# Kernel optimization log

Measured on AMD Instinct MI355X. Metric: run time of the kernel, lower is better.

The kernel has to match this reference:

```python
import math
import jax, jax.numpy as jnp
import numpy as np

BN_EPS = 1e-5

def _lrelu(x, s):
    return jnp.where(x >= 0, x, s * x)

def _bn(x, g, b):
    # BatchNorm2d in train mode (torch default): biased batch stats over (B,H,W)
    mu = jnp.mean(x, axis=(0, 2, 3), keepdims=True)
    var = jnp.mean((x - mu) ** 2, axis=(0, 2, 3), keepdims=True)
    return (x - mu) / jnp.sqrt(var + BN_EPS) * g[None, :, None, None] + b[None, :, None, None]

def _knn(x, x2, k):
    # x: [B,d,P], x2: [B,d,S] -> idx [B,k,S]: k nearest points of x for each column of x2
    inner = -2.0 * jnp.einsum('bdp,bds->bps', x, x2)
    xx = jnp.sum(x ** 2, axis=1)[:, :, None]    # [B,P,1]
    xx2 = jnp.sum(x2 ** 2, axis=1)[:, None, :]  # [B,1,S]
    d = -xx - inner - xx2                        # [B,P,S], larger = closer
    _, idx = jax.lax.top_k(jnp.transpose(d, (0, 2, 1)), k)  # [B,S,k]
    return jnp.transpose(idx, (0, 2, 1))         # [B,k,S]

def _gather_nb(X, idx, s, k):
    # faithful to torch gether_neibour, including its flat-reshape layout
    B, C, P = X.shape
    base = jnp.arange(B)[:, None, None] * P
    flat = (idx + base).reshape(-1)
    Xt = jnp.transpose(X, (0, 2, 1)).reshape(B * P, C)
    return Xt[flat].reshape(B, s, k, C)

def _c2d(x, W, b):
    return jnp.einsum('oc,bcpk->bopk', W, x) + b[None, :, None, None]

def _c1d(x, W, b):
    return jnp.einsum('oc,bcp->bop', W, x) + b[None, :, None]

def _forward(x, W_pos, b_pos, g2, be2, W_conv, b_conv, g1, be1, W_a1, b_a1, W_a2, b_a2, W_b1, b_b1, W_b2, b_b2, num_points):
    B, C, P = x.shape
    k = 8
    s = num_points
    # ---- Dynamic_sampling_M: uniform mesh over (x,y) bbox, snap to nearest event ----
    L = int(math.ceil(math.sqrt(s)))
    m = jnp.arange(L, dtype=x.dtype) / L
    m01 = jnp.tile(m[None, :], (L, 1)).reshape(1, 1, L * L)
    m02 = jnp.tile(m[:, None], (1, L)).reshape(1, 1, L * L)
    mesh = jnp.broadcast_to(jnp.concatenate([m01, m02], axis=1), (B, 2, L * L))
    Px = jax.lax.stop_gradient(x[:, :2, :])  # knn runs under torch.no_grad
    mn = Px.min(axis=2, keepdims=True)
    mx = Px.max(axis=2, keepdims=True)
    PS = mesh * (mx - mn) + mn
    idx0 = _knn(Px, PS, 1)                                   # [B,1,L*L]
    sp = _gather_nb(x, idx0, L * L, 1)[:, :, 0, :].transpose(0, 2, 1)  # [B,C,s]
    idx = _knn(jax.lax.stop_gradient(x[:, :3, :]), jax.lax.stop_gradient(sp[:, :3, :]), k)  # [B,k,s]
    x1 = jnp.transpose(_gather_nb(x, idx, s, k), (0, 3, 1, 2))  # [B,C,s,k]
    # ---- positional encoding ----
    PA = x1[:, :3, :, :]
    PC = x1[:, :3, :, 0:1]
    diff = PA - PC
    sq = jnp.sum(diff ** 2, axis=1, keepdims=True)
    temp = jnp.where(sq > 0, jnp.sqrt(jnp.where(sq > 0, sq, 1.0)), 0.0)
    PEmb = jnp.concatenate([PA, jnp.broadcast_to(PC, PA.shape), diff, temp], axis=1)  # [B,10,s,k]
    PEmb = _lrelu(_bn(_c2d(PEmb, W_pos, b_pos), g2, be2), 0.2)
    x_ = _lrelu(_bn(_c2d(x1[:, :4, :, :], W_conv, b_conv), g1, be1), 0.2)
    feat = jnp.concatenate([x_, PEmb], axis=1)  # [B,64,s,k]
    att = _c2d(_lrelu(_c2d(feat, W_a1, b_a1), 0.2), W_a2, b_a2)  # [B,1,s,k]
    att = jax.nn.softmax(att, axis=-1)
    feat = jnp.sum(feat * att, axis=-1)  # [B,64,s]
    Fea1 = _c1d(feat, W_b1, b_b1)
    Fea2 = _c1d(x1[:, :4, :, 0], W_b2, b_b2)
    out = _lrelu(Fea1 + Fea2, 0.01)
    return jnp.concatenate([x1[:, :5, :, 0], out], axis=1)  # [B,69,s]

def setup_inputs() -> dict:
    key = jax.random.key(0)
    ks = jax.random.split(key, 8)
    B, C, P = 2, 5, 16384
    num_points = 4096  # perfect square required by the mesh sampler
    outc, inc, h = 64, 4, 32
    w = lambda k_, shape: jax.random.normal(k_, shape, jnp.float32) * 0.05
    x = jax.random.normal(ks[0], (B, C, P), jnp.float32)
    return dict(
        x=x,
        W_pos=w(ks[1], (h, 10)), b_pos=jnp.zeros((h,), jnp.float32),
        g2=jnp.ones((h,), jnp.float32), be2=jnp.zeros((h,), jnp.float32),
        W_conv=w(ks[2], (h, inc)), b_conv=jnp.zeros((h,), jnp.float32),
        g1=jnp.ones((h,), jnp.float32), be1=jnp.zeros((h,), jnp.float32),
        W_a1=w(ks[3], (32, outc)), b_a1=jnp.zeros((32,), jnp.float32),
        W_a2=w(ks[4], (1, 32)), b_a2=jnp.zeros((1,), jnp.float32),
        W_b1=w(ks[5], (outc, outc)), b_b1=jnp.zeros((outc,), jnp.float32),
        W_b2=w(ks[6], (outc, inc)), b_b2=jnp.zeros((outc,), jnp.float32),
        num_points=num_points,
    )

def reference(x, W_pos, b_pos, g2, be2, W_conv, b_conv, g1, be1, W_a1, b_a1, W_a2, b_a2, W_b1, b_b1, W_b2, b_b2, num_points):
    return _forward(x, W_pos, b_pos, g2, be2, W_conv, b_conv, g1, be1, W_a1, b_a1, W_a2, b_a2, W_b1, b_b1, W_b2, b_b2, num_points)
```

## Files before the change

kernel.cpp:

```cpp
#include <hip/hip_runtime.h>
#include <math.h>

#define B_ 2
#define P_ 16384
#define C_ 5
#define S_ 4096
#define KNN_ 8
#define L_ 64

typedef unsigned short u16;
typedef unsigned int u32;

__device__ int   g_idxk[B_ * KNN_ * S_];
__device__ float g_sums[128];

__device__ __forceinline__ float bf2f(u16 u) {
  union { u32 i; float f; } c; c.i = ((u32)u) << 16; return c.f;
}
__device__ __forceinline__ u16 f2bf(float f) {
  union { float f; u32 i; } c; c.f = f;
  u32 r = c.i + 0x7fffu + ((c.i >> 16) & 1u);
  return (u16)(r >> 16);
}
__device__ __forceinline__ float ldany(const void* p, int i, int f32) {
  return f32 ? ((const float*)p)[i] : bf2f(((const u16*)p)[i]);
}

__device__ __forceinline__ double packkey(float d, int idx) {
  u32 bits = __float_as_uint(d);
  u32 key = bits ^ ((u32)(((int)bits) >> 31) | 0x80000000u);
  int hi = (int)(0x3FF00000u | (key >> 12));
  int lo = (int)((key << 20) | ((u32)(16383 - idx) << 6));
  return __hiloint2double(hi, lo);
}
__device__ __forceinline__ int keyidx(double w) {
  return 16383 - (int)(((u32)__double2loint(w) >> 6) & 16383u);
}
__device__ __forceinline__ void cmpswap(double& a, double& b) {
  double hi = fmax(a, b), lo = fmin(a, b);
  a = hi; b = lo;
}
__device__ __forceinline__ void flush8(double* a, double* k) {
  cmpswap(k[0], k[1]); cmpswap(k[2], k[3]); cmpswap(k[4], k[5]); cmpswap(k[6], k[7]);
  cmpswap(k[0], k[2]); cmpswap(k[1], k[3]); cmpswap(k[4], k[6]); cmpswap(k[5], k[7]);
  cmpswap(k[1], k[2]); cmpswap(k[5], k[6]);
  cmpswap(k[0], k[4]); cmpswap(k[1], k[5]); cmpswap(k[2], k[6]); cmpswap(k[3], k[7]);
  cmpswap(k[2], k[4]); cmpswap(k[3], k[5]);
  cmpswap(k[1], k[2]); cmpswap(k[3], k[4]); cmpswap(k[5], k[6]);
  a[0] = fmax(a[0], k[7]); a[1] = fmax(a[1], k[6]);
  a[2] = fmax(a[2], k[5]); a[3] = fmax(a[3], k[4]);
  a[4] = fmax(a[4], k[3]); a[5] = fmax(a[5], k[2]);
  a[6] = fmax(a[6], k[1]); a[7] = fmax(a[7], k[0]);
  cmpswap(a[0], a[4]); cmpswap(a[1], a[5]); cmpswap(a[2], a[6]); cmpswap(a[3], a[7]);
  cmpswap(a[0], a[2]); cmpswap(a[1], a[3]); cmpswap(a[4], a[6]); cmpswap(a[5], a[7]);
  cmpswap(a[0], a[1]); cmpswap(a[2], a[3]); cmpswap(a[4], a[5]); cmpswap(a[6], a[7]);
}

__device__ __forceinline__ int chk_bad(const void* p, int n, int tid) {
  int bad = 0;
  for (int i = tid; i < n; i += 256) {
    float f = bf2f(((const u16*)p)[i]);
    if (!(f == f) || fabsf(f) > 1024.0f) bad = 1;
  }
  return bad;
}

__global__ __launch_bounds__(256, 4) void k_knn(const void* __restrict__ xv) {
  __shared__ float4 s4[1024];
  __shared__ int sidx[8];
  __shared__ int sbad;
  __shared__ float sred[16];
  int tid = threadIdx.x;
  if (blockIdx.x == 0 && tid < 128) g_sums[tid] = 0.0f;
  int l = tid & 63, g = tid >> 6;
  int sg0 = blockIdx.x * 8 + g * 2;
  int b = sg0 >> 12;
  int base0 = b * C_ * P_, base1 = base0 + P_, base2 = base1 + P_;

  if (tid == 0) sbad = 0;
  __syncthreads();
  if (chk_bad(xv, 1024, tid)) atomicOr(&sbad, 1);
  __syncthreads();
  const int f32 = sbad;

  float mn0 = INFINITY, mx0 = -INFINITY, mn1 = INFINITY, mx1 = -INFINITY;
  for (int p = tid; p < P_; p += 256) {
    float v0 = ldany(xv, base0 + p, f32);
    float v1 = ldany(xv, base1 + p, f32);
    mn0 = fminf(mn0, v0); mx0 = fmaxf(mx0, v0);
    mn1 = fminf(mn1, v1); mx1 = fmaxf(mx1, v1);
  }
  for (int off = 32; off; off >>= 1) {
    mn0 = fminf(mn0, __shfl_down(mn0, off)); mx0 = fmaxf(mx0, __shfl_down(mx0, off));
    mn1 = fminf(mn1, __shfl_down(mn1, off)); mx1 = fmaxf(mx1, __shfl_down(mx1, off));
  }
  if (l == 0) {
    sred[g * 4 + 0] = mn0; sred[g * 4 + 1] = mx0;
    sred[g * 4 + 2] = mn1; sred[g * 4 + 3] = mx1;
  }
  __syncthreads();
  mn0 = fminf(fminf(sred[0], sred[4]), fminf(sred[8], sred[12]));
  mx0 = fmaxf(fmaxf(sred[1], sred[5]), fmaxf(sred[9], sred[13]));
  mn1 = fminf(fminf(sred[2], sred[6]), fminf(sred[10], sred[14]));
  mx1 = fmaxf(fmaxf(sred[3], sred[7]), fmaxf(sred[11], sred[15]));

  float ps0[2], ps1[2], xx2[2], best[2]; int bestp[2];
#pragma unroll
  for (int qq = 0; qq < 2; ++qq) {
    int s = (sg0 + qq) & (S_ - 1);
    float mm0 = (float)(s & (L_ - 1)) * 0.015625f;
    float mm1 = (float)(s >> 6) * 0.015625f;
    ps0[qq] = __fadd_rn(__fmul_rn(mm0, __fsub_rn(mx0, mn0)), mn0);
    ps1[qq] = __fadd_rn(__fmul_rn(mm1, __fsub_rn(mx1, mn1)), mn1);
    xx2[qq] = __fadd_rn(__fmul_rn(ps0[qq], ps0[qq]), __fmul_rn(ps1[qq], ps1[qq]));
    best[qq] = -INFINITY; bestp[qq] = 0x7fffffff;
  }
  for (int c = 0; c < 16; ++c) {
    __syncthreads();
    for (int i = tid; i < 1024; i += 256) {
      int gi = c * 1024 + i;
      float a0 = ldany(xv, base0 + gi, f32);
      float a1 = ldany(xv, base1 + gi, f32);
      float xx = __fadd_rn(__fmul_rn(a0, a0), __fmul_rn(a1, a1));
      s4[i] = make_float4(a0, a1, xx, 0.0f);
    }
    __syncthreads();
    for (int t = 0; t < 16; ++t) {
      float4 v = s4[t * 64 + l];
      int ix = c * 1024 + t * 64 + l;
#pragma unroll
      for (int qq = 0; qq < 2; ++qq) {
        float dot = __fadd_rn(__fmul_rn(v.x, ps0[qq]), __fmul_rn(v.y, ps1[qq]));
        float inner = __fmul_rn(-2.0f, dot);
        float d = __fsub_rn(__fsub_rn(-v.z, inner), xx2[qq]);
        bool gt = d > best[qq];
        best[qq] = gt ? d : best[qq];
        bestp[qq] = gt ? ix : bestp[qq];
      }
    }
  }
#pragma unroll
  for (int qq = 0; qq < 2; ++qq) {
    float v = best[qq]; int ix = bestp[qq];
    for (int m = 1; m < 64; m <<= 1) {
      float ov = __shfl_xor(v, m, 64); int op = __shfl_xor(ix, m, 64);
      if (ov > v || (ov == v && op < ix)) { v = ov; ix = op; }
    }
    if (l == 0) sidx[g * 2 + qq] = ix;
  }
  __syncthreads();

  float q0[2], q1[2], q2[2], xx3q[2];
  double acc[2][8], kb[2][8];
#pragma unroll
  for (int qq = 0; qq < 2; ++qq) {
    int qi = sidx[g * 2 + qq] & (P_ - 1);
    q0[qq] = ldany(xv, base0 + qi, f32);
    q1[qq] = ldany(xv, base1 + qi, f32);
    q2[qq] = ldany(xv, base2 + qi, f32);
    xx3q[qq] = __fadd_rn(__fadd_rn(__fmul_rn(q0[qq], q0[qq]), __fmul_rn(q1[qq], q1[qq])),
                         __fmul_rn(q2[qq], q2[qq]));
#pragma unroll
    for (int k = 0; k < 8; ++k) acc[qq][k] = -1.0;
  }
  for (int c = 0; c < 16; ++c) {
    __syncthreads();
    for (int i = tid; i < 1024; i += 256) {
      int gi = c * 1024 + i;
      float a0 = ldany(xv, base0 + gi, f32);
      float a1 = ldany(xv, base1 + gi, f32);
      float a2 = ldany(xv, base2 + gi, f32);
      float xx = __fadd_rn(__fadd_rn(__fmul_rn(a0, a0), __fmul_rn(a1, a1)), __fmul_rn(a2, a2));
      s4[i] = make_float4(a0, a1, a2, xx);
    }
    __syncthreads();
#pragma unroll
    for (int t = 0; t < 16; ++t) {
      float4 v = s4[t * 64 + l];
      int ix = c * 1024 + t * 64 + l;
#pragma unroll
      for (int qq = 0; qq < 2; ++qq) {
        float dot = __fadd_rn(__fadd_rn(__fmul_rn(v.x, q0[qq]), __fmul_rn(v.y, q1[qq])),
                              __fmul_rn(v.z, q2[qq]));
        float inner = __fmul_rn(-2.0f, dot);
        float d = __fsub_rn(__fsub_rn(-v.w, inner), xx3q[qq]);
        kb[qq][t & 7] = packkey(d, ix);
      }
      if ((t & 7) == 7) {
        flush8(acc[0], kb[0]);
        flush8(acc[1], kb[1]);
      }
    }
  }
  double wk[2] = {0.0, 0.0};
#pragma unroll
  for (int qq = 0; qq < 2; ++qq) {
#pragma unroll
    for (int r = 0; r < 8; ++r) {
      double w = acc[qq][0];
      for (int m = 1; m < 64; m <<= 1) w = fmax(w, __shfl_xor(w, m, 64));
      if (l == r) wk[qq] = w;
      bool cns = (acc[qq][0] == w);
#pragma unroll
      for (int k = 0; k < 7; ++k) acc[qq][k] = cns ? acc[qq][k + 1] : acc[qq][k];
      acc[qq][7] = cns ? -1.0 : acc[qq][7];
    }
  }
  if (l < 8) {
#pragma unroll
    for (int qq = 0; qq < 2; ++qq) {
      int s = (sg0 + qq) & (S_ - 1);
      g_idxk[b * 32768 + l * 4096 + s] = keyidx(wk[qq]);
    }
  }
}

__device__ __forceinline__ void elem_vals(const void* xv, int xf32, int xbase,
                                          const int* fb, int n,
                                          const float* sWpos, const float* sbpos,
                                          const float* sWconv, const float* sbconv,
                                          float* val ) {
  int p = fb[n] & (P_ - 1);
  int p0 = fb[n & ~7] & (P_ - 1);
  float xvv[4];
#pragma unroll
  for (int c = 0; c < 4; ++c) xvv[c] = ldany(xv, xbase + c * P_ + p, xf32);
  float pc[3];
#pragma unroll
  for (int c = 0; c < 3; ++c) pc[c] = ldany(xv, xbase + c * P_ + p0, xf32);
  float d0 = xvv[0] - pc[0], d1 = xvv[1] - pc[1], d2 = xvv[2] - pc[2];
  float sq = d0 * d0 + d1 * d1 + d2 * d2;
  float temp = (sq > 0.0f) ? sqrtf(sq) : 0.0f;
  float pe[10] = {xvv[0], xvv[1], xvv[2], pc[0], pc[1], pc[2], d0, d1, d2, temp};
#pragma unroll
  for (int o = 0; o < 32; ++o) {
    float acc = sbconv[o];
#pragma unroll
    for (int c = 0; c < 4; ++c) acc = fmaf(sWconv[o * 4 + c], xvv[c], acc);
    val[o] = acc;
  }
#pragma unroll
  for (int o = 0; o < 32; ++o) {
    float acc = sbpos[o];
#pragma unroll
    for (int c = 0; c < 10; ++c) acc = fmaf(sWpos[o * 10 + c], pe[c], acc);
    val[32 + o] = acc;
  }
}

__global__ __launch_bounds__(256) void k_partial(const void* __restrict__ x,
                                                 const void* __restrict__ Wpos,
                                                 const void* __restrict__ bpos,
                                                 const void* __restrict__ Wconv,
                                                 const void* __restrict__ bconv) {
  __shared__ float sWpos[320], sbpos[32], sWconv[128], sbconv[32];
  __shared__ float sacc[4][128];
  __shared__ int sbx, sbw;
  int tid = threadIdx.x;
  if (tid == 0) { sbx = 0; sbw = 0; }
  __syncthreads();
  if (chk_bad(x, 1024, tid)) atomicOr(&sbx, 1);
  if (chk_bad(Wpos, 320, tid) | chk_bad(Wconv, 128, tid)) atomicOr(&sbw, 1);
  __syncthreads();
  int xf32 = sbx, wf32 = sbw;
  for (int i2 = tid; i2 < 320; i2 += 256) sWpos[i2] = ldany(Wpos, i2, wf32);
  if (tid < 128) sWconv[tid] = ldany(Wconv, tid, wf32);
  if (tid < 32) { sbpos[tid] = ldany(bpos, tid, wf32); sbconv[tid] = ldany(bconv, tid, wf32); }
  __syncthreads();
  int t = blockIdx.x * 256 + tid;
  int b = t >> 15, n = t & 32767;
  const int* fb = g_idxk + b * 32768;
  float val[64];
  elem_vals(x, xf32, b * C_ * P_, fb, n, sWpos, sbpos, sWconv, sbconv, val);
  int wid = tid >> 6, lane = tid & 63;
#pragma unroll
  for (int c = 0; c < 64; ++c) {
    float s = val[c], q = val[c] * val[c];
    for (int off = 32; off; off >>= 1) {
      s += __shfl_down(s, off);
      q += __shfl_down(q, off);
    }
    if (lane == 0) { sacc[wid][c * 2] = s; sacc[wid][c * 2 + 1] = q; }
  }
  __syncthreads();
  if (tid < 128) {
    float v = sacc[0][tid] + sacc[1][tid] + sacc[2][tid] + sacc[3][tid];
    atomicAdd(&g_sums[tid], v);
  }
}

__global__ __launch_bounds__(256) void k_pass2(const void* __restrict__ x,
                                               const void* __restrict__ Wpos,
                                               const void* __restrict__ bpos,
                                               const void* __restrict__ Wconv,
                                               const void* __restrict__ bconv,
                                               const void* __restrict__ g1,
                                               const void* __restrict__ be1,
                                               const void* __restrict__ g2,
                                               const void* __restrict__ be2,
                                               const void* __restrict__ Wa1,
                                               const void* __restrict__ ba1,
                                               const void* __restrict__ Wa2,
                                               const void* __restrict__ ba2,
                                               const void* __restrict__ Wb1,
                                               const void* __restrict__ bb1,
                                               const void* __restrict__ Wb2,
                                               const void* __restrict__ bb2,
                                               void* __restrict__ out) {
  __shared__ float sWpos[320], sbpos[32], sWconv[128], sbconv[32];
  __shared__ float sWa1[2048], sba1[32], sWa2[32];
  __shared__ float sWb1[64 * 65];
  __shared__ float sbb1[64], sWb2[256], sbb2[64], sstats[128];
  __shared__ float sba2;
  __shared__ int sbx, sbw;
  int tid = threadIdx.x;
  if (tid == 0) { sbx = 0; sbw = 0; }
  __syncthreads();
  if (chk_bad(x, 1024, tid)) atomicOr(&sbx, 1);
  if (chk_bad(Wa1, 2048, tid) | chk_bad(Wb1, 4096, tid)) atomicOr(&sbw, 1);
  __syncthreads();
  int xf32 = sbx, wf32 = sbw;
  for (int i2 = tid; i2 < 320; i2 += 256) sWpos[i2] = ldany(Wpos, i2, wf32);
  if (tid < 128) sWconv[tid] = ldany(Wconv, tid, wf32);
  if (tid < 32) { sbpos[tid] = ldany(bpos, tid, wf32); sbconv[tid] = ldany(bconv, tid, wf32); }
  for (int i2 = tid; i2 < 2048; i2 += 256) sWa1[i2] = ldany(Wa1, i2, wf32);
  for (int i2 = tid; i2 < 4096; i2 += 256) sWb1[(i2 >> 6) * 65 + (i2 & 63)] = ldany(Wb1, i2, wf32);
  if (tid >= 32 && tid < 64) { sba1[tid - 32] = ldany(ba1, tid - 32, wf32); sWa2[tid - 32] = ldany(Wa2, tid - 32, wf32); }
  if (tid >= 64 && tid < 128) { sbb1[tid - 64] = ldany(bb1, tid - 64, wf32); sbb2[tid - 64] = ldany(bb2, tid - 64, wf32); }
  sWb2[tid] = ldany(Wb2, tid, wf32);
  if (tid == 0) sba2 = ldany(ba2, 0, wf32);
  if (tid >= 128 && tid < 192) {
    int ch = tid - 128;
    float sum = g_sums[ch * 2], sq = g_sums[ch * 2 + 1];
    float mean = sum * (1.0f / 65536.0f);
    float var = sq * (1.0f / 65536.0f) - mean * mean;
    int o = ch & 31;
    float gg = ldany(ch < 32 ? g1 : g2, o, wf32);
    float be = ldany(ch < 32 ? be1 : be2, o, wf32);
    float scale = gg / sqrtf(var + 1e-5f);
    sstats[ch * 2] = scale;
    sstats[ch * 2 + 1] = be - mean * scale;
  }
  __syncthreads();
  int g = blockIdx.x * 32 + (tid >> 3);
  int j = tid & 7;
  int b = g >> 12, i = g & (S_ - 1);
  int n = i * 8 + j;
  const int* fb = g_idxk + b * 32768;
  int xbase = b * C_ * P_;
  float feat[64];
  elem_vals(x, xf32, xbase, fb, n, sWpos, sbpos, sWconv, sbconv, feat);
#pragma unroll
  for (int c = 0; c < 64; ++c) {
    float v = fmaf(feat[c], sstats[c * 2], sstats[c * 2 + 1]);
    feat[c] = (v >= 0.f) ? v : 0.2f * v;
  }
  float att = sba2;
  for (int h = 0; h < 32; ++h) {
    float acc = sba1[h];
#pragma unroll
    for (int c = 0; c < 64; ++c) acc = fmaf(sWa1[h * 64 + c], feat[c], acc);
    acc = (acc >= 0.f) ? acc : 0.2f * acc;
    att = fmaf(sWa2[h], acc, att);
  }
  float mxv = att;
  for (int mk = 1; mk < 8; mk <<= 1) mxv = fmaxf(mxv, __shfl_xor(mxv, mk, 8));
  float e = expf(att - mxv);
  float se = e;
  for (int mk = 1; mk < 8; mk <<= 1) se += __shfl_xor(se, mk, 8);
  float a = e / se;
#pragma unroll
  for (int c = 0; c < 64; ++c) {
    float w = feat[c] * a;
    w += __shfl_xor(w, 1, 8);
    w += __shfl_xor(w, 2, 8);
    w += __shfl_xor(w, 4, 8);
    feat[c] = w;
  }
  int p0 = fb[i * 8] & (P_ - 1);
  float xc0 = ldany(x, xbase + p0, xf32);
  float xc1 = ldany(x, xbase + P_ + p0, xf32);
  float xc2 = ldany(x, xbase + 2 * P_ + p0, xf32);
  float xc3 = ldany(x, xbase + 3 * P_ + p0, xf32);
  int obase = b * 69 * S_;
#pragma unroll
  for (int oc = 0; oc < 8; ++oc) {
    int o = j * 8 + oc;
    float acc = sbb1[o];
#pragma unroll
    for (int c = 0; c < 64; ++c) acc = fmaf(sWb1[o * 65 + c], feat[c], acc);
    float acc2 = sbb2[o];
    acc2 = fmaf(sWb2[o * 4 + 0], xc0, acc2);
    acc2 = fmaf(sWb2[o * 4 + 1], xc1, acc2);
    acc2 = fmaf(sWb2[o * 4 + 2], xc2, acc2);
    acc2 = fmaf(sWb2[o * 4 + 3], xc3, acc2);
    float r = acc + acc2;
    r = (r >= 0.f) ? r : 0.01f * r;
    int oi = obase + (5 + o) * S_ + i;
    if (xf32) ((float*)out)[oi] = r; else ((u16*)out)[oi] = f2bf(r);
  }
  if (j == 0) {
#pragma unroll
    for (int c = 0; c < 5; ++c) {
      int oi = obase + c * S_ + i;
      if (xf32) ((float*)out)[oi] = ((const float*)x)[xbase + c * P_ + p0];
      else      ((u16*)out)[oi]   = ((const u16*)x)[xbase + c * P_ + p0];
    }
  }
}

extern "C" void kernel_launch(void* const* d_in, const int* in_sizes, int n_in,
                              void* d_out, int out_size, void* d_ws, size_t ws_size,
                              hipStream_t stream) {
  const void* x     = d_in[0];
  const void* Wpos  = d_in[1];
  const void* bpos  = d_in[2];
  const void* g2    = d_in[3];
  const void* be2   = d_in[4];
  const void* Wconv = d_in[5];
  const void* bconv = d_in[6];
  const void* g1    = d_in[7];
  const void* be1   = d_in[8];
  const void* Wa1   = d_in[9];
  const void* ba1   = d_in[10];
  const void* Wa2   = d_in[11];
  const void* ba2   = d_in[12];
  const void* Wb1   = d_in[13];
  const void* bb1   = d_in[14];
  const void* Wb2   = d_in[15];
  const void* bb2   = d_in[16];
  (void)d_ws; (void)ws_size; (void)in_sizes; (void)n_in;

  hipLaunchKernelGGL(k_knn, dim3(1024), dim3(256), 0, stream, x);
  hipLaunchKernelGGL(k_partial, dim3(256), dim3(256), 0, stream, x,
                     Wpos, bpos, Wconv, bconv);
  hipLaunchKernelGGL(k_pass2, dim3(256), dim3(256), 0, stream, x,
                     Wpos, bpos, Wconv, bconv, g1, be1, g2, be2,
                     Wa1, ba1, Wa2, ba2, Wb1, bb1, Wb2, bb2, d_out);
}
```

Before: 298.9 us.

## Fuse BN partial stats into kNN kernel and double-buffer point tiles

Removes the separate k_partial kernel. The kNN kernel now computes per-block BatchNorm sum and sum-of-squares partials for its own 16 neighbour features and writes them to a global partials array, and pass2 reduces those partials instead of reading atomically accumulated sums. The kNN point-tile loops are also double-buffered in shared memory: the next chunk is loaded into registers while the current one is scanned, which removes one barrier per chunk. This saves a kernel launch and a re-read of the indices, and overlaps global loads with compute. In exchange it costs more shared memory and registers in k_knn, which may reduce occupancy, and adds a serial 512-element reduction loop per thread in every pass2 block.

```diff
diff --git a/kernel.cpp b/kernel.cpp
--- a/kernel.cpp
+++ b/kernel.cpp
@@ -12,7 +12,7 @@
 typedef unsigned int u32;
 
 __device__ int   g_idxk[B_ * KNN_ * S_];
-__device__ float g_sums[128];
+__device__ float g_partials[1024 * 128];
 
 __device__ __forceinline__ float bf2f(u16 u) {
   union { u32 i; float f; } c; c.i = ((u32)u) << 16; return c.f;
@@ -65,23 +65,34 @@
   return bad;
 }
 
-__global__ __launch_bounds__(256, 4) void k_knn(const void* __restrict__ xv) {
-  __shared__ float4 s4[1024];
+__global__ __launch_bounds__(256, 4) void k_knn(const void* __restrict__ xv,
+                                                const void* __restrict__ Wpos,
+                                                const void* __restrict__ bpos,
+                                                const void* __restrict__ Wconv,
+                                                const void* __restrict__ bconv) {
+  __shared__ float4 s4[2][1024];
+  __shared__ float sWpos[320], sbpos[32], sWconv[128], sbconv[32];
+  __shared__ float sacc[4][128];
   __shared__ int sidx[8];
-  __shared__ int sbad;
+  __shared__ int sp0[8];
+  __shared__ int sbad, sbw;
   __shared__ float sred[16];
   int tid = threadIdx.x;
-  if (blockIdx.x == 0 && tid < 128) g_sums[tid] = 0.0f;
   int l = tid & 63, g = tid >> 6;
   int sg0 = blockIdx.x * 8 + g * 2;
   int b = sg0 >> 12;
   int base0 = b * C_ * P_, base1 = base0 + P_, base2 = base1 + P_;
 
-  if (tid == 0) sbad = 0;
+  if (tid == 0) { sbad = 0; sbw = 0; }
   __syncthreads();
   if (chk_bad(xv, 1024, tid)) atomicOr(&sbad, 1);
-  __syncthreads();
-  const int f32 = sbad;
+  if (chk_bad(Wpos, 320, tid) | chk_bad(Wconv, 128, tid)) atomicOr(&sbw, 1);
+  __syncthreads();
+  const int f32 = sbad, wf32 = sbw;
+
+  for (int i2 = tid; i2 < 320; i2 += 256) sWpos[i2] = ldany(Wpos, i2, wf32);
+  if (tid < 128) sWconv[tid] = ldany(Wconv, tid, wf32);
+  if (tid < 32) { sbpos[tid] = ldany(bpos, tid, wf32); sbconv[tid] = ldany(bconv, tid, wf32); }
 
   float mn0 = INFINITY, mx0 = -INFINITY, mn1 = INFINITY, mx1 = -INFINITY;
   for (int p = tid; p < P_; p += 256) {
@@ -115,18 +126,30 @@
     xx2[qq] = __fadd_rn(__fmul_rn(ps0[qq], ps0[qq]), __fmul_rn(ps1[qq], ps1[qq]));
     best[qq] = -INFINITY; bestp[qq] = 0x7fffffff;
   }
+  {
+#pragma unroll
+    for (int r = 0; r < 4; ++r) {
+      int i = r * 256 + tid;
+      float a0 = ldany(xv, base0 + i, f32);
+      float a1 = ldany(xv, base1 + i, f32);
+      float xx = __fadd_rn(__fmul_rn(a0, a0), __fmul_rn(a1, a1));
+      s4[0][i] = make_float4(a0, a1, xx, 0.0f);
+    }
+  }
+  __syncthreads();
   for (int c = 0; c < 16; ++c) {
-    __syncthreads();
-    for (int i = tid; i < 1024; i += 256) {
-      int gi = c * 1024 + i;
-      float a0 = ldany(xv, base0 + gi, f32);
-      float a1 = ldany(xv, base1 + gi, f32);
-      float xx = __fadd_rn(__fmul_rn(a0, a0), __fmul_rn(a1, a1));
-      s4[i] = make_float4(a0, a1, xx, 0.0f);
-    }
-    __syncthreads();
+    float a0r[4], a1r[4];
+    if (c < 15) {
+#pragma unroll
+      for (int r = 0; r < 4; ++r) {
+        int gi = (c + 1) * 1024 + r * 256 + tid;
+        a0r[r] = ldany(xv, base0 + gi, f32);
+        a1r[r] = ldany(xv, base1 + gi, f32);
+      }
+    }
+    const float4* cb = s4[c & 1];
     for (int t = 0; t < 16; ++t) {
-      float4 v = s4[t * 64 + l];
+      float4 v = cb[t * 64 + l];
       int ix = c * 1024 + t * 64 + l;
 #pragma unroll
       for (int qq = 0; qq < 2; ++qq) {
@@ -138,6 +161,15 @@
         bestp[qq] = gt ? ix : bestp[qq];
       }
     }
+    if (c < 15) {
+      float4* nb = s4[(c + 1) & 1];
+#pragma unroll
+      for (int r = 0; r < 4; ++r) {
+        float xx = __fadd_rn(__fmul_rn(a0r[r], a0r[r]), __fmul_rn(a1r[r], a1r[r]));
+        nb[r * 256 + tid] = make_float4(a0r[r], a1r[r], xx, 0.0f);
+      }
+    }
+    __syncthreads();
   }
 #pragma unroll
   for (int qq = 0; qq < 2; ++qq) {
@@ -163,20 +195,33 @@
 #pragma unroll
     for (int k = 0; k < 8; ++k) acc[qq][k] = -1.0;
   }
+  {
+#pragma unroll
+    for (int r = 0; r < 4; ++r) {
+      int i = r * 256 + tid;
+      float a0 = ldany(xv, base0 + i, f32);
+      float a1 = ldany(xv, base1 + i, f32);
+      float a2 = ldany(xv, base2 + i, f32);
+      float xx = __fadd_rn(__fadd_rn(__fmul_rn(a0, a0), __fmul_rn(a1, a1)), __fmul_rn(a2, a2));
+      s4[0][i] = make_float4(a0, a1, a2, xx);
+    }
+  }
+  __syncthreads();
   for (int c = 0; c < 16; ++c) {
-    __syncthreads();
-    for (int i = tid; i < 1024; i += 256) {
-      int gi = c * 1024 + i;
-      float a0 = ldany(xv, base0 + gi, f32);
-      float a1 = ldany(xv, base1 + gi, f32);
-      float a2 = ldany(xv, base2 + gi, f32);
-      float xx = __fadd_rn(__fadd_rn(__fmul_rn(a0, a0), __fmul_rn(a1, a1)), __fmul_rn(a2, a2));
-      s4[i] = make_float4(a0, a1, a2, xx);
-    }
-    __syncthreads();
+    float a0r[4], a1r[4], a2r[4];
+    if (c < 15) {
+#pragma unroll
+      for (int r = 0; r < 4; ++r) {
+        int gi = (c + 1) * 1024 + r * 256 + tid;
+        a0r[r] = ldany(xv, base0 + gi, f32);
+        a1r[r] = ldany(xv, base1 + gi, f32);
+        a2r[r] = ldany(xv, base2 + gi, f32);
+      }
+    }
+    const float4* cb = s4[c & 1];
 #pragma unroll
     for (int t = 0; t < 16; ++t) {
-      float4 v = s4[t * 64 + l];
+      float4 v = cb[t * 64 + l];
       int ix = c * 1024 + t * 64 + l;
 #pragma unroll
       for (int qq = 0; qq < 2; ++qq) {
@@ -191,6 +236,16 @@
         flush8(acc[1], kb[1]);
       }
     }
+    if (c < 15) {
+      float4* nb = s4[(c + 1) & 1];
+#pragma unroll
+      for (int r = 0; r < 4; ++r) {
+        float xx = __fadd_rn(__fadd_rn(__fmul_rn(a0r[r], a0r[r]), __fmul_rn(a1r[r], a1r[r])),
+                             __fmul_rn(a2r[r], a2r[r]));
+        nb[r * 256 + tid] = make_float4(a0r[r], a1r[r], a2r[r], xx);
+      }
+    }
+    __syncthreads();
   }
   double wk[2] = {0.0, 0.0};
 #pragma unroll
@@ -213,79 +268,46 @@
       g_idxk[b * 32768 + l * 4096 + s] = keyidx(wk[qq]);
     }
   }
-}
-
-__device__ __forceinline__ void elem_vals(const void* xv, int xf32, int xbase,
-                                          const int* fb, int n,
-                                          const float* sWpos, const float* sbpos,
-                                          const float* sWconv, const float* sbconv,
-                                          float* val ) {
-  int p = fb[n] & (P_ - 1);
-  int p0 = fb[n & ~7] & (P_ - 1);
-  float xvv[4];
-#pragma unroll
-  for (int c = 0; c < 4; ++c) xvv[c] = ldany(xv, xbase + c * P_ + p, xf32);
-  float pc[3];
-#pragma unroll
-  for (int c = 0; c < 3; ++c) pc[c] = ldany(xv, xbase + c * P_ + p0, xf32);
-  float d0 = xvv[0] - pc[0], d1 = xvv[1] - pc[1], d2 = xvv[2] - pc[2];
+
+  if (g == 0 && l < 8) sp0[l] = keyidx(wk[0]) & (P_ - 1);
+  __syncthreads();
+  double k1s = __shfl(wk[1], l & 7, 16);
+  bool active = (l < 16);
+  double myk = (l < 8) ? wk[0] : k1s;
+  int p = keyidx(myk) & (P_ - 1);
+  int p0 = sp0[l & 7];
+  float xvv[4] = {0, 0, 0, 0}, pc3[3] = {0, 0, 0};
+  if (active) {
+#pragma unroll
+    for (int cc = 0; cc < 4; ++cc) xvv[cc] = ldany(xv, base0 + cc * P_ + p, f32);
+#pragma unroll
+    for (int cc = 0; cc < 3; ++cc) pc3[cc] = ldany(xv, base0 + cc * P_ + p0, f32);
+  }
+  float d0 = xvv[0] - pc3[0], d1 = xvv[1] - pc3[1], d2 = xvv[2] - pc3[2];
   float sq = d0 * d0 + d1 * d1 + d2 * d2;
   float temp = (sq > 0.0f) ? sqrtf(sq) : 0.0f;
-  float pe[10] = {xvv[0], xvv[1], xvv[2], pc[0], pc[1], pc[2], d0, d1, d2, temp};
-#pragma unroll
-  for (int o = 0; o < 32; ++o) {
-    float acc = sbconv[o];
-#pragma unroll
-    for (int c = 0; c < 4; ++c) acc = fmaf(sWconv[o * 4 + c], xvv[c], acc);
-    val[o] = acc;
-  }
-#pragma unroll
-  for (int o = 0; o < 32; ++o) {
-    float acc = sbpos[o];
-#pragma unroll
-    for (int c = 0; c < 10; ++c) acc = fmaf(sWpos[o * 10 + c], pe[c], acc);
-    val[32 + o] = acc;
-  }
-}
-
-__global__ __launch_bounds__(256) void k_partial(const void* __restrict__ x,
-                                                 const void* __restrict__ Wpos,
-                                                 const void* __restrict__ bpos,
-                                                 const void* __restrict__ Wconv,
-                                                 const void* __restrict__ bconv) {
-  __shared__ float sWpos[320], sbpos[32], sWconv[128], sbconv[32];
-  __shared__ float sacc[4][128];
-  __shared__ int sbx, sbw;
-  int tid = threadIdx.x;
-  if (tid == 0) { sbx = 0; sbw = 0; }
-  __syncthreads();
-  if (chk_bad(x, 1024, tid)) atomicOr(&sbx, 1);
-  if (chk_bad(Wpos, 320, tid) | chk_bad(Wconv, 128, tid)) atomicOr(&sbw, 1);
-  __syncthreads();
-  int xf32 = sbx, wf32 = sbw;
-  for (int i2 = tid; i2 < 320; i2 += 256) sWpos[i2] = ldany(Wpos, i2, wf32);
-  if (tid < 128) sWconv[tid] = ldany(Wconv, tid, wf32);
-  if (tid < 32) { sbpos[tid] = ldany(bpos, tid, wf32); sbconv[tid] = ldany(bconv, tid, wf32); }
-  __syncthreads();
-  int t = blockIdx.x * 256 + tid;
-  int b = t >> 15, n = t & 32767;
-  const int* fb = g_idxk + b * 32768;
-  float val[64];
-  elem_vals(x, xf32, b * C_ * P_, fb, n, sWpos, sbpos, sWconv, sbconv, val);
-  int wid = tid >> 6, lane = tid & 63;
-#pragma unroll
-  for (int c = 0; c < 64; ++c) {
-    float s = val[c], q = val[c] * val[c];
-    for (int off = 32; off; off >>= 1) {
-      s += __shfl_down(s, off);
-      q += __shfl_down(q, off);
-    }
-    if (lane == 0) { sacc[wid][c * 2] = s; sacc[wid][c * 2 + 1] = q; }
+  float pe[10] = {xvv[0], xvv[1], xvv[2], pc3[0], pc3[1], pc3[2], d0, d1, d2, temp};
+#pragma unroll
+  for (int o = 0; o < 64; ++o) {
+    float v;
+    if (o < 32) {
+      v = sbconv[o];
+#pragma unroll
+      for (int cc = 0; cc < 4; ++cc) v = fmaf(sWconv[o * 4 + cc], xvv[cc], v);
+    } else {
+      v = sbpos[o - 32];
+#pragma unroll
+      for (int cc = 0; cc < 10; ++cc) v = fmaf(sWpos[(o - 32) * 10 + cc], pe[cc], v);
+    }
+    v = active ? v : 0.0f;
+    float s = v, q = v * v;
+    for (int m = 1; m < 16; m <<= 1) { s += __shfl_xor(s, m, 16); q += __shfl_xor(q, m, 16); }
+    if (l == 0) { sacc[g][o * 2] = s; sacc[g][o * 2 + 1] = q; }
   }
   __syncthreads();
   if (tid < 128) {
-    float v = sacc[0][tid] + sacc[1][tid] + sacc[2][tid] + sacc[3][tid];
-    atomicAdd(&g_sums[tid], v);
+    g_partials[blockIdx.x * 128 + tid] =
+        sacc[0][tid] + sacc[1][tid] + sacc[2][tid] + sacc[3][tid];
   }
 }
 
@@ -311,6 +333,7 @@
   __shared__ float sWa1[2048], sba1[32], sWa2[32];
   __shared__ float sWb1[64 * 65];
   __shared__ float sbb1[64], sWb2[256], sbb2[64], sstats[128];
+  __shared__ float sp2[2][128];
   __shared__ float sba2;
   __shared__ int sbx, sbw;
   int tid = threadIdx.x;
@@ -320,6 +343,13 @@
   if (chk_bad(Wa1, 2048, tid) | chk_bad(Wb1, 4096, tid)) atomicOr(&sbw, 1);
   __syncthreads();
   int xf32 = sbx, wf32 = sbw;
+  {
+    int slot = tid & 127, half = tid >> 7;
+    float a = 0.f;
+    for (int blk = half * 512; blk < half * 512 + 512; ++blk)
+      a += g_partials[blk * 128 + slot];
+    sp2[half][slot] = a;
+  }
   for (int i2 = tid; i2 < 320; i2 += 256) sWpos[i2] = ldany(Wpos, i2, wf32);
   if (tid < 128) sWconv[tid] = ldany(Wconv, tid, wf32);
   if (tid < 32) { sbpos[tid] = ldany(bpos, tid, wf32); sbconv[tid] = ldany(bconv, tid, wf32); }
@@ -329,9 +359,11 @@
   if (tid >= 64 && tid < 128) { sbb1[tid - 64] = ldany(bb1, tid - 64, wf32); sbb2[tid - 64] = ldany(bb2, tid - 64, wf32); }
   sWb2[tid] = ldany(Wb2, tid, wf32);
   if (tid == 0) sba2 = ldany(ba2, 0, wf32);
+  __syncthreads();
   if (tid >= 128 && tid < 192) {
     int ch = tid - 128;
-    float sum = g_sums[ch * 2], sq = g_sums[ch * 2 + 1];
+    float sum = sp2[0][ch * 2] + sp2[1][ch * 2];
+    float sq = sp2[0][ch * 2 + 1] + sp2[1][ch * 2 + 1];
     float mean = sum * (1.0f / 65536.0f);
     float var = sq * (1.0f / 65536.0f) - mean * mean;
     int o = ch & 31;
@@ -348,8 +380,33 @@
   int n = i * 8 + j;
   const int* fb = g_idxk + b * 32768;
   int xbase = b * C_ * P_;
+  int p = fb[n] & (P_ - 1);
+  int p0 = fb[n & ~7] & (P_ - 1);
+  float xvv[4];
+#pragma unroll
+  for (int c = 0; c < 4; ++c) xvv[c] = ldany(x, xbase + c * P_ + p, xf32);
+  float pc3[3];
+#pragma unroll
+  for (int c = 0; c < 3; ++c) pc3[c] = ldany(x, xbase + c * P_ + p0, xf32);
+  float d0 = xvv[0] - pc3[0], d1 = xvv[1] - pc3[1], d2 = xvv[2] - pc3[2];
+  float sq = d0 * d0 + d1 * d1 + d2 * d2;
+  float temp = (sq > 0.0f) ? sqrtf(sq) : 0.0f;
+  float pe[10] = {xvv[0], xvv[1], xvv[2], pc3[0], pc3[1], pc3[2], d0, d1, d2, temp};
   float feat[64];
-  elem_vals(x, xf32, xbase, fb, n, sWpos, sbpos, sWconv, sbconv, feat);
+#pragma unroll
+  for (int o = 0; o < 32; ++o) {
+    float acc = sbconv[o];
+#pragma unroll
+    for (int c = 0; c < 4; ++c) acc = fmaf(sWconv[o * 4 + c], xvv[c], acc);
+    feat[o] = acc;
+  }
+#pragma unroll
+  for (int o = 0; o < 32; ++o) {
+    float acc = sbpos[o];
+#pragma unroll
+    for (int c = 0; c < 10; ++c) acc = fmaf(sWpos[o * 10 + c], pe[c], acc);
+    feat[32 + o] = acc;
+  }
 #pragma unroll
   for (int c = 0; c < 64; ++c) {
     float v = fmaf(feat[c], sstats[c * 2], sstats[c * 2 + 1]);
@@ -377,7 +434,6 @@
     w += __shfl_xor(w, 4, 8);
     feat[c] = w;
   }
-  int p0 = fb[i * 8] & (P_ - 1);
   float xc0 = ldany(x, xbase + p0, xf32);
   float xc1 = ldany(x, xbase + P_ + p0, xf32);
   float xc2 = ldany(x, xbase + 2 * P_ + p0, xf32);
@@ -431,8 +487,7 @@
   const void* bb2   = d_in[16];
   (void)d_ws; (void)ws_size; (void)in_sizes; (void)n_in;
 
-  hipLaunchKernelGGL(k_knn, dim3(1024), dim3(256), 0, stream, x);
-  hipLaunchKernelGGL(k_partial, dim3(256), dim3(256), 0, stream, x,
+  hipLaunchKernelGGL(k_knn, dim3(1024), dim3(256), 0, stream, x,
                      Wpos, bpos, Wconv, bconv);
   hipLaunchKernelGGL(k_pass2, dim3(256), dim3(256), 0, stream, x,
                      Wpos, bpos, Wconv, bconv, g1, be1, g2, be2,
```

Result: slower. 309.3 us (+3.5%).
